# Performance work log

Hardware: AMD Instinct MI355X
Metric: run time of the kernel (lower is better)

Reference implementation:

```python
import jax, jax.numpy as jnp
import numpy as np

NUM_EXPERTS = 8
TOP_K = 2
N_EMBD = 1024
D_FFN = 2048  # 4*n_embd // top_k, already block-aligned


def setup_inputs() -> dict:
    key = jax.random.key(0)
    k1, k2, k3, k4 = jax.random.split(key, 4)
    x = jax.random.normal(k1, (4, 2048, N_EMBD), jnp.float32)
    w_router = jax.random.normal(k2, (N_EMBD, NUM_EXPERTS), jnp.float32) * 0.02
    w1 = jax.random.normal(k3, (N_EMBD, D_FFN * NUM_EXPERTS), jnp.float32) * 0.02
    w2 = jax.random.normal(k4, (D_FFN * NUM_EXPERTS, N_EMBD), jnp.float32) * 0.02
    return {"x": x, "w_router": w_router, "w1": w1, "w2": w2}


def reference(x, w_router, w1, w2):
    B, S, D = x.shape
    T = B * S
    xf = x.reshape(T, D)

    # --- routing ---
    logits = xf @ w_router                                   # [T, E]
    probs = jax.nn.softmax(logits.astype(jnp.float32), axis=-1)
    topw, topi = jax.lax.top_k(probs, TOP_K)                 # [T, K]
    topw = topw / topw.sum(-1, keepdims=True)                # norm_topk_prob
    topw = topw.astype(x.dtype)

    # dense combine weights [T, E]: router weight where selected, else 0
    wd = jnp.zeros((T, NUM_EXPERTS), x.dtype)
    wd = wd.at[jnp.arange(T)[:, None], topi].add(topw)

    # --- grouped (per-expert) GEMM; source has NO nonlinearity between w1/w2 ---
    w1r = w1.reshape(D, NUM_EXPERTS, D_FFN)   # column layout is expert-major
    w2r = w2.reshape(NUM_EXPERTS, D_FFN, D)
    out = jnp.zeros((T, D), x.dtype)
    for e in range(NUM_EXPERTS):
        h = xf @ w1r[:, e, :]                 # [T, F]
        out = out + wd[:, e:e+1] * (h @ w2r[e])
    out = out.reshape(B, S, D)

    # --- aux losses ---
    router_z_loss = jnp.mean(
        jax.scipy.special.logsumexp(logits.astype(jnp.float32), axis=-1) ** 2)
    p_i = probs.mean(axis=0)                                  # [E]
    f_i = jnp.zeros(NUM_EXPERTS, x.dtype).at[topi.reshape(-1)].add(
        jnp.asarray(1.0 / (T * TOP_K), x.dtype))
    load_balance_loss = NUM_EXPERTS * (f_i @ p_i.astype(x.dtype))
    return out, router_z_loss, load_balance_loss, f_i
```

## Files before the change

kernel.cpp:

```cpp
#include <hip/hip_runtime.h>
#include <hip/hip_bf16.h>
#include <stdint.h>
#include <stddef.h>


typedef unsigned short ushort_t;
typedef __attribute__((ext_vector_type(8))) short short8;
typedef __attribute__((ext_vector_type(4))) float floatx4;

#define T_TOK 8192
#define NE    8
#define DD    1024
#define FF    2048
#define W1ROW (NE * FF)

#define BM 128
#define BN 128
#define BK 64

typedef const __attribute__((address_space(1))) unsigned int gas_u32;
typedef __attribute__((address_space(3)))       unsigned int las_u32;
#define GLOAD16(gp, lp) \
  __builtin_amdgcn_global_load_lds((gas_u32*)(gp), (las_u32*)(lp), 16, 0, 0)

__device__ __forceinline__ unsigned short f2bf(float f) {
  union { float f; unsigned u; } c; c.f = f;
  unsigned r = c.u + 0x7fffu + ((c.u >> 16) & 1u);
  return (unsigned short)(r >> 16);
}
__device__ __forceinline__ unsigned packbf2(float a, float b) {
  unsigned ua = __float_as_uint(a) + 0x8000u;
  unsigned ub = __float_as_uint(b) + 0x8000u;
  return __builtin_amdgcn_perm(ub, ua, 0x07060302);
}

static const size_t OFF_CNT   = 0;
static const size_t OFF_ZPART = 256;
static const size_t OFF_PPART = 512;
static const size_t OFF_REXP  = 4096;
static const size_t OFF_RWTS  = 36864;
static const size_t OFF_IDS   = 102400;
static const size_t OFF_WTS   = 364544;
static const size_t OFF_W2T   = 1048576;
static const size_t OFF_MT    = OFF_W2T + 33554432;
static const size_t OFF_XB    = OFF_W2T;

__global__ __launch_bounds__(256)
void router_kernel(const float* __restrict__ x, const float* __restrict__ wrt,
                   unsigned* __restrict__ rexp, float2* __restrict__ rwts,
                   float* __restrict__ zpart, float* __restrict__ ppart) {
  int w = threadIdx.x >> 6, ln = threadIdx.x & 63;
  int t = blockIdx.x * 4 + w;
  const float* xr = x + (size_t)t * DD;
  float acc[8] = {0.f, 0.f, 0.f, 0.f, 0.f, 0.f, 0.f, 0.f};
  for (int i = 0; i < 16; ++i) {
    int d = ln + (i << 6);
    float xv = xr[d];
    float4 r0 = *(const float4*)(wrt + (size_t)d * 8);
    float4 r1 = *(const float4*)(wrt + (size_t)d * 8 + 4);
    acc[0] += xv * r0.x;  acc[1] += xv * r0.y;
    acc[2] += xv * r0.z;  acc[3] += xv * r0.w;
    acc[4] += xv * r1.x;  acc[5] += xv * r1.y;
    acc[6] += xv * r1.z;  acc[7] += xv * r1.w;
  }
#pragma unroll
  for (int e = 0; e < 8; ++e) {
#pragma unroll
    for (int off = 32; off > 0; off >>= 1) acc[e] += __shfl_xor(acc[e], off, 64);
  }
  if (ln == 0) {
    float m = acc[0];
#pragma unroll
    for (int e = 1; e < 8; ++e) m = fmaxf(m, acc[e]);
    float p[8], s = 0.f;
#pragma unroll
    for (int e = 0; e < 8; ++e) { p[e] = expf(acc[e] - m); s += p[e]; }
    float z = m + logf(s);
    int e1 = 0; float v1 = acc[0];
#pragma unroll
    for (int e = 1; e < 8; ++e) if (acc[e] > v1) { v1 = acc[e]; e1 = e; }
    int e2 = (e1 == 0) ? 1 : 0; float v2 = acc[e2];
#pragma unroll
    for (int e = 0; e < 8; ++e) if (e != e1 && acc[e] > v2) { v2 = acc[e]; e2 = e; }
    float p1 = p[e1], p2 = p[e2];
    float inv = 1.f / (p1 + p2);
    rexp[t] = (unsigned)e1 | ((unsigned)e2 << 8);
    rwts[t] = make_float2(p1 * inv, p2 * inv);
    int sh = blockIdx.x & 63;
    unsafeAtomicAdd(&zpart[sh], z * z);
    float sinv = 1.f / s;
#pragma unroll
    for (int e = 0; e < 8; ++e) unsafeAtomicAdd(&ppart[sh * 8 + e], p[e] * sinv);
  }
}

__global__ __launch_bounds__(256)
void build_lists_kernel(const unsigned* __restrict__ rexp, const float2* __restrict__ rwts,
                        int* __restrict__ cnt, int* __restrict__ ids, float* __restrict__ wts) {
  __shared__ int lcnt[8];
  __shared__ int lbase[8];
  if (threadIdx.x < 8) lcnt[threadIdx.x] = 0;
  __syncthreads();
  int t = blockIdx.x * 256 + threadIdx.x;
  unsigned re = rexp[t];
  float2 w = rwts[t];
  int e1 = (int)(re & 0xffu), e2 = (int)((re >> 8) & 0xffu);
  int p1 = atomicAdd(&lcnt[e1], 1);
  int p2 = atomicAdd(&lcnt[e2], 1);
  __syncthreads();
  if (threadIdx.x < 8) lbase[threadIdx.x] = atomicAdd(&cnt[threadIdx.x], lcnt[threadIdx.x]);
  __syncthreads();
  int i1 = e1 * T_TOK + lbase[e1] + p1;
  ids[i1] = t;  wts[i1] = w.x;
  int i2 = e2 * T_TOK + lbase[e2] + p2;
  ids[i2] = t;  wts[i2] = w.y;
}

__global__ __launch_bounds__(256)
void transpose_w2_kernel(const float* __restrict__ w2, ushort_t* __restrict__ W2T) {
  __shared__ ushort_t tile[64 * 72];
  int e = blockIdx.z, f0 = blockIdx.x * 64, j0 = blockIdx.y * 64;
  int tid = (int)threadIdx.x;
  int r = tid >> 2, c0 = (tid & 3) * 16;
  const float* src = w2 + ((size_t)(e * FF + f0 + r)) * DD + j0 + c0;
  float4 v0 = *(const float4*)(src);
  float4 v1 = *(const float4*)(src + 4);
  float4 v2 = *(const float4*)(src + 8);
  float4 v3 = *(const float4*)(src + 12);
  uint4 pa = make_uint4(packbf2(v0.x, v0.y), packbf2(v0.z, v0.w),
                        packbf2(v1.x, v1.y), packbf2(v1.z, v1.w));
  uint4 pb = make_uint4(packbf2(v2.x, v2.y), packbf2(v2.z, v2.w),
                        packbf2(v3.x, v3.y), packbf2(v3.z, v3.w));
  *(uint4*)&tile[r * 72 + c0]     = pa;
  *(uint4*)&tile[r * 72 + c0 + 8] = pb;
  __syncthreads();
  int j = tid >> 2, g0 = (tid & 3) * 16;
  ushort_t o[16];
#pragma unroll
  for (int i = 0; i < 16; ++i) o[i] = tile[(g0 + i) * 72 + j];
  ushort_t* dst = W2T + ((size_t)(e * DD + j0 + j)) * FF + f0 + g0;
  *(uint4*)(dst)     = *(uint4*)&o[0];
  *(uint4*)(dst + 8) = *(uint4*)&o[8];
}

__global__ __launch_bounds__(256)
void convert_x_kernel(const float* __restrict__ x, ushort_t* __restrict__ XB) {
  size_t i = ((size_t)blockIdx.x * 256 + threadIdx.x) * 8;
  float4 f0 = *(const float4*)(x + i);
  float4 f1 = *(const float4*)(x + i + 4);
  uint4 pk = make_uint4(packbf2(f0.x, f0.y), packbf2(f0.z, f0.w),
                        packbf2(f1.x, f1.y), packbf2(f1.z, f1.w));
  *(uint4*)(XB + i) = pk;
}

__global__ __launch_bounds__(256)
void gemm_mt_kernel(const ushort_t* __restrict__ W2T, const float* __restrict__ w1,
                    ushort_t* __restrict__ MT) {
  int e  = blockIdx.x;
  int m0 = blockIdx.y * BM;
  int n0 = blockIdx.z * BN;
  __shared__ alignas(16) ushort_t As[BM * BK];
  __shared__ alignas(16) ushort_t Bs[BN * BK];
  const ushort_t* Abase = W2T + (size_t)e * DD * FF;
  int tid = (int)threadIdx.x;
  int w = tid >> 6, ln = tid & 63;
  int wr = w >> 1, wc = w & 1;
  int mrow = ln & 15, kq = ln >> 4;
  const ushort_t* agp[4];
#pragma unroll
  for (int it = 0; it < 4; ++it) {
    int r  = w * 32 + it * 8 + (ln >> 3);
    int cs = (ln & 7) ^ (r & 7);
    agp[it] = Abase + (size_t)(m0 + r) * FF + cs * 8;
  }
  floatx4 acc[4][4] = {};
  for (int k0 = 0; k0 < FF; k0 += BK) {
    __syncthreads();
#pragma unroll
    for (int it = 0; it < 4; ++it)
      GLOAD16(agp[it] + k0, &As[(w * 32 + it * 8) * BK]);
#pragma unroll
    for (int it = 0; it < 4; ++it) {
      int c = it * 256 + tid;
      int r = c >> 3, b = c & 7;
      const float* p = w1 + (size_t)(n0 + r) * W1ROW + e * FF + k0 + b * 8;
      float4 f0 = *(const float4*)(p);
      float4 f1 = *(const float4*)(p + 4);
      uint4 pk = make_uint4(packbf2(f0.x, f0.y), packbf2(f0.z, f0.w),
                            packbf2(f1.x, f1.y), packbf2(f1.z, f1.w));
      *(uint4*)&Bs[r * BK + ((b ^ (r & 7)) << 3)] = pk;
    }
    __syncthreads();
#pragma unroll
    for (int s = 0; s < 2; ++s) {
      short8 fa[4], fb[4];
#pragma unroll
      for (int i = 0; i < 4; ++i) {
        int r = wr * 64 + i * 16 + mrow;
        fa[i] = *(const short8*)&As[r * BK + ((((s << 2) | kq) ^ (r & 7)) << 3)];
      }
#pragma unroll
      for (int j = 0; j < 4; ++j) {
        int r = wc * 64 + j * 16 + mrow;
        fb[j] = *(const short8*)&Bs[r * BK + ((((s << 2) | kq) ^ (r & 7)) << 3)];
      }
#pragma unroll
      for (int i = 0; i < 4; ++i)
#pragma unroll
        for (int j = 0; j < 4; ++j)
          acc[i][j] = __builtin_amdgcn_mfma_f32_16x16x32_bf16(fa[i], fb[j], acc[i][j], 0, 0, 0);
    }
  }
  ushort_t* outp = MT + (size_t)e * DD * DD;
#pragma unroll
  for (int i = 0; i < 4; ++i) {
#pragma unroll
    for (int j = 0; j < 4; ++j) {
#pragma unroll
      for (int rr = 0; rr < 4; ++rr) {
        int m = m0 + wr * 64 + i * 16 + kq * 4 + rr;
        int n = n0 + wc * 64 + j * 16 + mrow;
        outp[(size_t)m * DD + n] = f2bf(acc[i][j][rr]);
      }
    }
  }
}

__global__ __launch_bounds__(256)
void gemm_moe_kernel(const ushort_t* __restrict__ XB, const ushort_t* __restrict__ MT,
                     const int* __restrict__ cnt, const int* __restrict__ ids,
                     const float* __restrict__ wts, float* __restrict__ outp) {
  int e = blockIdx.x;
  int ce = cnt[e];
  int s0 = blockIdx.y * BM;
  if (s0 >= ce) return;
  int n0 = blockIdx.z * BN;
  __shared__ int   rid_l[BM];
  __shared__ float wrow[BM];
  __shared__ alignas(16) ushort_t As[BM * BK];
  __shared__ alignas(16) ushort_t Bs[BN * BK];
  int tid = (int)threadIdx.x;
  if (tid < BM) {
    int s = s0 + tid;
    if (s < ce) { rid_l[tid] = ids[e * T_TOK + s]; wrow[tid] = wts[e * T_TOK + s]; }
    else        { rid_l[tid] = 0;                  wrow[tid] = 0.f; }
  }
  __syncthreads();
  const ushort_t* Bbase = MT + (size_t)e * DD * DD;
  int w = tid >> 6, ln = tid & 63;
  int wr = w >> 1, wc = w & 1;
  int mrow = ln & 15, kq = ln >> 4;
  const ushort_t* agp[4];
  const ushort_t* bgp[4];
#pragma unroll
  for (int it = 0; it < 4; ++it) {
    int r  = w * 32 + it * 8 + (ln >> 3);
    int cs = (ln & 7) ^ (r & 7);
    int tok = rid_l[r];
    agp[it] = XB + (size_t)tok * DD + cs * 8;
    bgp[it] = Bbase + (size_t)(n0 + r) * DD + cs * 8;
  }
  floatx4 acc[4][4] = {};
  for (int k0 = 0; k0 < DD; k0 += BK) {
    __syncthreads();
#pragma unroll
    for (int it = 0; it < 4; ++it)
      GLOAD16(agp[it] + k0, &As[(w * 32 + it * 8) * BK]);
#pragma unroll
    for (int it = 0; it < 4; ++it)
      GLOAD16(bgp[it] + k0, &Bs[(w * 32 + it * 8) * BK]);
    __syncthreads();
#pragma unroll
    for (int s = 0; s < 2; ++s) {
      short8 fa[4], fb[4];
#pragma unroll
      for (int i = 0; i < 4; ++i) {
        int r = wr * 64 + i * 16 + mrow;
        fa[i] = *(const short8*)&As[r * BK + ((((s << 2) | kq) ^ (r & 7)) << 3)];
      }
#pragma unroll
      for (int j = 0; j < 4; ++j) {
        int r = wc * 64 + j * 16 + mrow;
        fb[j] = *(const short8*)&Bs[r * BK + ((((s << 2) | kq) ^ (r & 7)) << 3)];
      }
#pragma unroll
      for (int i = 0; i < 4; ++i)
#pragma unroll
        for (int j = 0; j < 4; ++j)
          acc[i][j] = __builtin_amdgcn_mfma_f32_16x16x32_bf16(fa[i], fb[j], acc[i][j], 0, 0, 0);
    }
  }
#pragma unroll
  for (int i = 0; i < 4; ++i) {
#pragma unroll
    for (int j = 0; j < 4; ++j) {
#pragma unroll
      for (int rr = 0; rr < 4; ++rr) {
        int mloc = wr * 64 + i * 16 + kq * 4 + rr;
        if (s0 + mloc < ce) {
          int tok = rid_l[mloc];
          int ncol = n0 + wc * 64 + j * 16 + mrow;
          unsafeAtomicAdd(&outp[(size_t)tok * DD + ncol], acc[i][j][rr] * wrow[mloc]);
        }
      }
    }
  }
}

__global__ void losses_kernel(const float* __restrict__ zpart, const float* __restrict__ ppart,
                              const int* __restrict__ cnt, float* __restrict__ outaux) {
  if (threadIdx.x == 0) {
    float z = 0.f;
    for (int i = 0; i < 64; ++i) z += zpart[i];
    z /= (float)T_TOK;
    float p[8];
    for (int e = 0; e < 8; ++e) {
      float s = 0.f;
      for (int b = 0; b < 64; ++b) s += ppart[b * 8 + e];
      p[e] = s / (float)T_TOK;
    }
    float lb = 0.f;
    for (int e = 0; e < 8; ++e) lb += ((float)cnt[e] / (float)(T_TOK * 2)) * p[e];
    lb *= (float)NE;
    outaux[0] = z;
    outaux[1] = lb;
    for (int e = 0; e < 8; ++e) outaux[2 + e] = (float)cnt[e] / (float)(T_TOK * 2);
  }
}

extern "C" void kernel_launch(void* const* d_in, const int* in_sizes, int n_in,
                              void* d_out, int out_size, void* d_ws, size_t ws_size,
                              hipStream_t stream) {
  const float* x   = (const float*)d_in[0];
  const float* wrt = (const float*)d_in[1];
  const float* w1  = (const float*)d_in[2];
  const float* w2  = (const float*)d_in[3];
  float* out = (float*)d_out;

  char* ws = (char*)d_ws;
  int*      cnt   = (int*)     (ws + OFF_CNT);
  float*    zpart = (float*)   (ws + OFF_ZPART);
  float*    ppart = (float*)   (ws + OFF_PPART);
  unsigned* rexp  = (unsigned*)(ws + OFF_REXP);
  float2*   rwts  = (float2*)  (ws + OFF_RWTS);
  int*      ids   = (int*)     (ws + OFF_IDS);
  float*    wtsf  = (float*)   (ws + OFF_WTS);
  ushort_t* W2T   = (ushort_t*)(ws + OFF_W2T);
  ushort_t* MT    = (ushort_t*)(ws + OFF_MT);
  ushort_t* XB    = (ushort_t*)(ws + OFF_XB);

  hipMemsetAsync(d_ws, 0, 4096, stream);
  hipMemsetAsync(d_out, 0, (size_t)out_size * 4, stream);
  router_kernel<<<T_TOK / 4, 256, 0, stream>>>(x, wrt, rexp, rwts, zpart, ppart);
  build_lists_kernel<<<T_TOK / 256, 256, 0, stream>>>(rexp, rwts, cnt, ids, wtsf);
  transpose_w2_kernel<<<dim3(FF / 64, DD / 64, NE), 256, 0, stream>>>(w2, W2T);
  gemm_mt_kernel<<<dim3(NE, DD / BM, DD / BN), 256, 0, stream>>>(W2T, w1, MT);
  convert_x_kernel<<<(T_TOK * DD) / (8 * 256), 256, 0, stream>>>(x, XB);
  gemm_moe_kernel<<<dim3(NE, T_TOK / BM, DD / BN), 256, 0, stream>>>(XB, MT, cnt, ids, wtsf, out);
  losses_kernel<<<1, 64, 0, stream>>>(zpart, ppart, cnt, out + (size_t)T_TOK * DD);
}
```

Before: 410.5 us.

## Double-buffer LDS tiles in both expert GEMM kernels to overlap loads

Both the fused weight-product GEMM and the routed token GEMM now use two LDS buffers. The next K-tile is prefetched, via direct-to-LDS loads or register loads that are packed to bf16 later, while MFMAs run on the current tile, which hides global memory latency. The MoE kernel also drops its shared-memory token-id and weight staging and reads the ids and weights straight from global memory in the prologue and epilogue. In exchange, LDS per block doubles, which can reduce occupancy, and the prefetched fp32 tiles raise register pressure.

```diff
diff --git a/kernel.cpp b/kernel.cpp
--- a/kernel.cpp
+++ b/kernel.cpp
@@ -159,8 +159,8 @@
   int e  = blockIdx.x;
   int m0 = blockIdx.y * BM;
   int n0 = blockIdx.z * BN;
-  __shared__ alignas(16) ushort_t As[BM * BK];
-  __shared__ alignas(16) ushort_t Bs[BN * BK];
+  __shared__ alignas(16) ushort_t As[2][BM * BK];
+  __shared__ alignas(16) ushort_t Bs[2][BN * BK];
   const ushort_t* Abase = W2T + (size_t)e * DD * FF;
   int tid = (int)threadIdx.x;
   int w = tid >> 6, ln = tid & 63;
@@ -173,42 +173,73 @@
     int cs = (ln & 7) ^ (r & 7);
     agp[it] = Abase + (size_t)(m0 + r) * FF + cs * 8;
   }
+  const float* bgp[4];
+  int brq[4];
+#pragma unroll
+  for (int it = 0; it < 4; ++it) {
+    int r = it * 32 + (tid >> 3), q = tid & 7;
+    bgp[it] = w1 + (size_t)(n0 + r) * W1ROW + e * FF + q * 8;
+    brq[it] = r * BK + ((q ^ (r & 7)) << 3);
+  }
+  float4 rb0[4], rb1[4];
+
+#define MT_ISSUE_A(t, b)                                              \
+  {  _Pragma("unroll")                                                \
+     for (int it = 0; it < 4; ++it)                                   \
+       GLOAD16(agp[it] + (t) * BK, &As[b][(w * 32 + it * 8) * BK]); }
+#define MT_LOAD_B(t)                                                  \
+  {  _Pragma("unroll")                                                \
+     for (int it = 0; it < 4; ++it) {                                 \
+       rb0[it] = *(const float4*)(bgp[it] + (t) * BK);                \
+       rb1[it] = *(const float4*)(bgp[it] + (t) * BK + 4); } }
+#define MT_PACK_B(b)                                                  \
+  {  _Pragma("unroll")                                                \
+     for (int it = 0; it < 4; ++it) {                                 \
+       uint4 pk = make_uint4(packbf2(rb0[it].x, rb0[it].y),           \
+                             packbf2(rb0[it].z, rb0[it].w),           \
+                             packbf2(rb1[it].x, rb1[it].y),           \
+                             packbf2(rb1[it].z, rb1[it].w));          \
+       *(uint4*)&Bs[b][brq[it]] = pk; } }
+
+  MT_ISSUE_A(0, 0);
+  MT_LOAD_B(0);
+  __syncthreads();
+  MT_PACK_B(0);
+  MT_ISSUE_A(1, 1);
+  MT_LOAD_B(1);
+  __syncthreads();
+
   floatx4 acc[4][4] = {};
-  for (int k0 = 0; k0 < FF; k0 += BK) {
-    __syncthreads();
-#pragma unroll
-    for (int it = 0; it < 4; ++it)
-      GLOAD16(agp[it] + k0, &As[(w * 32 + it * 8) * BK]);
-#pragma unroll
-    for (int it = 0; it < 4; ++it) {
-      int c = it * 256 + tid;
-      int r = c >> 3, b = c & 7;
-      const float* p = w1 + (size_t)(n0 + r) * W1ROW + e * FF + k0 + b * 8;
-      float4 f0 = *(const float4*)(p);
-      float4 f1 = *(const float4*)(p + 4);
-      uint4 pk = make_uint4(packbf2(f0.x, f0.y), packbf2(f0.z, f0.w),
-                            packbf2(f1.x, f1.y), packbf2(f1.z, f1.w));
-      *(uint4*)&Bs[r * BK + ((b ^ (r & 7)) << 3)] = pk;
-    }
-    __syncthreads();
+  const int NT = FF / BK;
+  for (int t = 0; t < NT; ++t) {
+    int b = t & 1;
 #pragma unroll
     for (int s = 0; s < 2; ++s) {
       short8 fa[4], fb[4];
 #pragma unroll
       for (int i = 0; i < 4; ++i) {
         int r = wr * 64 + i * 16 + mrow;
-        fa[i] = *(const short8*)&As[r * BK + ((((s << 2) | kq) ^ (r & 7)) << 3)];
+        fa[i] = *(const short8*)&As[b][r * BK + ((((s << 2) | kq) ^ (r & 7)) << 3)];
       }
 #pragma unroll
       for (int j = 0; j < 4; ++j) {
         int r = wc * 64 + j * 16 + mrow;
-        fb[j] = *(const short8*)&Bs[r * BK + ((((s << 2) | kq) ^ (r & 7)) << 3)];
+        fb[j] = *(const short8*)&Bs[b][r * BK + ((((s << 2) | kq) ^ (r & 7)) << 3)];
       }
 #pragma unroll
       for (int i = 0; i < 4; ++i)
 #pragma unroll
         for (int j = 0; j < 4; ++j)
           acc[i][j] = __builtin_amdgcn_mfma_f32_16x16x32_bf16(fa[i], fb[j], acc[i][j], 0, 0, 0);
+    }
+    if (t + 1 < NT) {
+      __syncthreads();
+      MT_PACK_B(b ^ 1);
+      __syncthreads();
+      if (t + 2 < NT) {
+        MT_ISSUE_A(t + 2, b);
+        MT_LOAD_B(t + 2);
+      }
     }
   }
   ushort_t* outp = MT + (size_t)e * DD * DD;
@@ -224,6 +255,9 @@
       }
     }
   }
+#undef MT_ISSUE_A
+#undef MT_LOAD_B
+#undef MT_PACK_B
 }
 
 __global__ __launch_bounds__(256)
@@ -235,17 +269,11 @@
   int s0 = blockIdx.y * BM;
   if (s0 >= ce) return;
   int n0 = blockIdx.z * BN;
-  __shared__ int   rid_l[BM];
-  __shared__ float wrow[BM];
-  __shared__ alignas(16) ushort_t As[BM * BK];
-  __shared__ alignas(16) ushort_t Bs[BN * BK];
+  __shared__ alignas(16) ushort_t As[2][BM * BK];
+  __shared__ alignas(16) ushort_t Bs[2][BN * BK];
   int tid = (int)threadIdx.x;
-  if (tid < BM) {
-    int s = s0 + tid;
-    if (s < ce) { rid_l[tid] = ids[e * T_TOK + s]; wrow[tid] = wts[e * T_TOK + s]; }
-    else        { rid_l[tid] = 0;                  wrow[tid] = 0.f; }
-  }
-  __syncthreads();
+  const int* idsE = ids + e * T_TOK + s0;
+  const float* wtsE = wts + e * T_TOK + s0;
   const ushort_t* Bbase = MT + (size_t)e * DD * DD;
   int w = tid >> 6, ln = tid & 63;
   int wr = w >> 1, wc = w & 1;
@@ -256,32 +284,39 @@
   for (int it = 0; it < 4; ++it) {
     int r  = w * 32 + it * 8 + (ln >> 3);
     int cs = (ln & 7) ^ (r & 7);
-    int tok = rid_l[r];
+    int tok = (s0 + r < ce) ? idsE[r] : 0;
     agp[it] = XB + (size_t)tok * DD + cs * 8;
     bgp[it] = Bbase + (size_t)(n0 + r) * DD + cs * 8;
   }
+
+#define MOE_ISSUE(t, b)                                                  \
+  {  _Pragma("unroll")                                                   \
+     for (int it = 0; it < 4; ++it)                                      \
+       GLOAD16(agp[it] + (t) * BK, &As[b][(w * 32 + it * 8) * BK]);      \
+     _Pragma("unroll")                                                   \
+     for (int it = 0; it < 4; ++it)                                      \
+       GLOAD16(bgp[it] + (t) * BK, &Bs[b][(w * 32 + it * 8) * BK]); }
+
+  MOE_ISSUE(0, 0);
+  __syncthreads();
+  MOE_ISSUE(1, 1);
+
   floatx4 acc[4][4] = {};
-  for (int k0 = 0; k0 < DD; k0 += BK) {
-    __syncthreads();
-#pragma unroll
-    for (int it = 0; it < 4; ++it)
-      GLOAD16(agp[it] + k0, &As[(w * 32 + it * 8) * BK]);
-#pragma unroll
-    for (int it = 0; it < 4; ++it)
-      GLOAD16(bgp[it] + k0, &Bs[(w * 32 + it * 8) * BK]);
-    __syncthreads();
+  const int NT = DD / BK;
+  for (int t = 0; t < NT; ++t) {
+    int b = t & 1;
 #pragma unroll
     for (int s = 0; s < 2; ++s) {
       short8 fa[4], fb[4];
 #pragma unroll
       for (int i = 0; i < 4; ++i) {
         int r = wr * 64 + i * 16 + mrow;
-        fa[i] = *(const short8*)&As[r * BK + ((((s << 2) | kq) ^ (r & 7)) << 3)];
+        fa[i] = *(const short8*)&As[b][r * BK + ((((s << 2) | kq) ^ (r & 7)) << 3)];
       }
 #pragma unroll
       for (int j = 0; j < 4; ++j) {
         int r = wc * 64 + j * 16 + mrow;
-        fb[j] = *(const short8*)&Bs[r * BK + ((((s << 2) | kq) ^ (r & 7)) << 3)];
+        fb[j] = *(const short8*)&Bs[b][r * BK + ((((s << 2) | kq) ^ (r & 7)) << 3)];
       }
 #pragma unroll
       for (int i = 0; i < 4; ++i)
@@ -289,22 +324,28 @@
         for (int j = 0; j < 4; ++j)
           acc[i][j] = __builtin_amdgcn_mfma_f32_16x16x32_bf16(fa[i], fb[j], acc[i][j], 0, 0, 0);
     }
+    if (t + 1 < NT) {
+      __syncthreads();
+      if (t + 2 < NT) MOE_ISSUE(t + 2, b);
+    }
   }
 #pragma unroll
   for (int i = 0; i < 4; ++i) {
 #pragma unroll
-    for (int j = 0; j < 4; ++j) {
-#pragma unroll
-      for (int rr = 0; rr < 4; ++rr) {
-        int mloc = wr * 64 + i * 16 + kq * 4 + rr;
-        if (s0 + mloc < ce) {
-          int tok = rid_l[mloc];
+    for (int rr = 0; rr < 4; ++rr) {
+      int mloc = wr * 64 + i * 16 + kq * 4 + rr;
+      if (s0 + mloc < ce) {
+        int   tok = idsE[mloc];
+        float wv  = wtsE[mloc];
+#pragma unroll
+        for (int j = 0; j < 4; ++j) {
           int ncol = n0 + wc * 64 + j * 16 + mrow;
-          unsafeAtomicAdd(&outp[(size_t)tok * DD + ncol], acc[i][j][rr] * wrow[mloc]);
+          unsafeAtomicAdd(&outp[(size_t)tok * DD + ncol], acc[i][j][rr] * wv);
         }
       }
     }
   }
+#undef MOE_ISSUE
 }
 
 __global__ void losses_kernel(const float* __restrict__ zpart, const float* __restrict__ ppart,
```

Result: no change. 416.6 us (+1.5%).
